# Kernel tuning notes

Hardware: AMD Instinct MI355X
Metric: run time of the kernel (lower is better)

## Reference

```python
import jax, jax.numpy as jnp
import numpy as np

NUM_USERS = 100000
NUM_ITEMS = 50000
NUM_EDGES = 4000000
EMB_DIM = 64
K_HOPS = 3


def setup_inputs() -> dict:
    key = jax.random.key(0)
    k1, k2, k3, k4, k5, k6 = jax.random.split(key, 6)
    N = NUM_USERS + NUM_ITEMS
    return {
        "users_emb": jax.random.normal(k1, (NUM_USERS, EMB_DIM), dtype=jnp.float32) * 0.1,
        "items_emb": jax.random.normal(k2, (NUM_ITEMS, EMB_DIM), dtype=jnp.float32) * 0.1,
        "edge_row": jax.random.randint(k3, (NUM_EDGES,), 0, N, dtype=jnp.int32),
        "edge_col": jax.random.randint(k4, (NUM_EDGES,), 0, N, dtype=jnp.int32),
        "user_id": jax.random.randint(k5, (4096,), 0, NUM_USERS, dtype=jnp.int32),
        "item_ids": jax.random.randint(k6, (4096,), 0, NUM_ITEMS, dtype=jnp.int32),
    }


def reference(users_emb, items_emb, edge_row, edge_col, user_id, item_ids):
    num_users = users_emb.shape[0]
    N = num_users + items_emb.shape[0]
    dt = users_emb.dtype

    # gcn_norm (no self loops): deg = rowsum of A, w_e = d_r^{-1/2} d_c^{-1/2}
    deg = jax.ops.segment_sum(jnp.ones(edge_row.shape[0], dtype=dt), edge_row,
                              num_segments=N)
    deg_inv_sqrt = jnp.where(deg > 0, 1.0 / jnp.sqrt(jnp.where(deg > 0, deg, 1.0)), 0.0)
    w = deg_inv_sqrt[edge_row] * deg_inv_sqrt[edge_col]  # [E]

    emb = jnp.concatenate([users_emb, items_emb], axis=0)  # [N, D]
    acc = emb  # running sum of K+1 layer snapshots
    for _ in range(K_HOPS):
        # SpMM: out[r] += w_e * emb[c]
        emb = jax.ops.segment_sum(w[:, None] * emb[edge_col], edge_row,
                                  num_segments=N)
        acc = acc + emb
    emb_final = acc / (K_HOPS + 1)  # layer-mean pooling

    users_final = emb_final[user_id]               # [B, D]
    items_final = emb_final[num_users + item_ids]  # [B, D]
    return jnp.concatenate([users_final, items_final], axis=1)  # [B, 2D]
```

## Files before the change

### kernel.cpp

```cpp
#include <hip/hip_runtime.h>
#include <hip/hip_bf16.h>

#define NUSERS 100000
#define NITEMS 50000
#define NN (NUSERS + NITEMS)
#define NE 4000000
#define DIM 64
#define BQ 4096
#define NBIN ((NN + 255) >> 8)
#define BINCAP 9216
#define EPB 4096

typedef unsigned short u16;
typedef unsigned int u32;
typedef float v2f __attribute__((ext_vector_type(2)));

__device__ __forceinline__ float bf2f(u16 u) {
    return __uint_as_float(((unsigned)u) << 16);
}
__device__ __forceinline__ u16 f2bf(float f) {
    unsigned x = __float_as_uint(f);
    return (u16)((x + 0x7FFFu + ((x >> 16) & 1u)) >> 16);
}
__device__ __forceinline__ void add8p(v2f* acc2, uint4 u) {
    acc2[0] += (v2f){__uint_as_float(u.x << 16), __uint_as_float(u.x & 0xffff0000u)};
    acc2[1] += (v2f){__uint_as_float(u.y << 16), __uint_as_float(u.y & 0xffff0000u)};
    acc2[2] += (v2f){__uint_as_float(u.z << 16), __uint_as_float(u.z & 0xffff0000u)};
    acc2[3] += (v2f){__uint_as_float(u.w << 16), __uint_as_float(u.w & 0xffff0000u)};
}
__device__ __forceinline__ uint4 ld_row(const char* __restrict__ base, int c, int dgoff) {
    u32 off = ((u32)c << 7) + (u32)dgoff;
    return *(const uint4*)(base + off);
}

__device__ __forceinline__ void rowsum_core(int start, int n8, int c_all,
                                            const int* __restrict__ col_s,
                                            const char* __restrict__ inb,
                                            int eslot, int dgoff, v2f* acc2) {
    int G = n8 >> 3;
    if (G <= 8) {
        int cg[8];
#pragma unroll
        for (int g = 0; g < 8; ++g)
            cg[g] = __shfl(c_all, (g << 3) + eslot, 64);
        uint4 v[8];
#pragma unroll
        for (int g = 0; g < 8; ++g)
            if (g < G) v[g] = ld_row(inb, cg[g], dgoff);
#pragma unroll
        for (int g = 0; g < 8; ++g)
            if (g < G) add8p(acc2, v[g]);
    } else {
        int i = eslot;
        int c0 = col_s[start + i];
        uint4 v0 = ld_row(inb, c0, dgoff);
        for (i += 8; i < n8; i += 8) {
            int c1 = col_s[start + i];
            uint4 v1 = ld_row(inb, c1, dgoff);
            add8p(acc2, v0);
            v0 = v1;
        }
        add8p(acc2, v0);
    }
}

__device__ __forceinline__ void reduce_acc(v2f* acc2) {
#pragma unroll
    for (int off = 8; off <= 32; off <<= 1)
#pragma unroll
        for (int j = 0; j < 4; ++j) {
            v2f o;
            o.x = __shfl_xor(acc2[j].x, off, 64);
            o.y = __shfl_xor(acc2[j].y, off, 64);
            acc2[j] += o;
        }
}

__global__ void k_init(int* __restrict__ bin_cur, u32* __restrict__ m2w,
                       u16* __restrict__ ea, u16* __restrict__ eb) {
    int t = blockIdx.x * blockDim.x + threadIdx.x;
    if (t < NBIN) bin_cur[t] = t * BINCAP;
    if (t < 37504) m2w[t] = 0;
    if (t < 32) {
        ((u32*)(ea + (size_t)NN * DIM))[t] = 0;
        ((u32*)(eb + (size_t)NN * DIM))[t] = 0;
    }
}

__global__ void k_binA(const int* __restrict__ row, const int* __restrict__ col,
                       int* __restrict__ bin_cur, u32* __restrict__ pairs, int E) {
    __shared__ int hist[NBIN];
    __shared__ int cbase[NBIN];
    int t = threadIdx.x;
    for (int b = t; b < NBIN; b += 256) hist[b] = 0;
    __syncthreads();
    int base = blockIdx.x * EPB;
    int r[16], c[16];
#pragma unroll
    for (int i = 0; i < 16; ++i) {
        int e = base + i * 256 + t;
        if (e < E) {
            r[i] = row[e];
            c[i] = col[e];
            atomicAdd(&hist[r[i] >> 8], 1);
        } else {
            r[i] = -1;
        }
    }
    __syncthreads();
    for (int b = t; b < NBIN; b += 256) {
        int h = hist[b];
        cbase[b] = (h > 0) ? atomicAdd(&bin_cur[b], h) : 0;
    }
    __syncthreads();
#pragma unroll
    for (int i = 0; i < 16; ++i) {
        if (r[i] >= 0) {
            int b = r[i] >> 8;
            int off = atomicSub(&hist[b], 1) - 1;
            pairs[(size_t)cbase[b] + off] = ((u32)(r[i] & 255) << 24) | (u32)c[i];
        }
    }
}

__global__ void k_binB(const u32* __restrict__ pairs, const int* __restrict__ bin_cur,
                       int* __restrict__ col_s, int* __restrict__ rs,
                       int* __restrict__ deg) {
    __shared__ int cnt[256];
    __shared__ int pscan[256];
    __shared__ int cur[256];
    int b = blockIdx.x;
    int t = threadIdx.x;
    int base = b * BINCAP;
    int end = bin_cur[b];
    cnt[t] = 0;
    __syncthreads();
    for (int i = base + t; i < end; i += 256)
        atomicAdd(&cnt[pairs[i] >> 24], 1);
    __syncthreads();
    int v = cnt[t];
    int pv = (v + 7) & ~7;
    pscan[t] = pv;
    __syncthreads();
    for (int off = 1; off < 256; off <<= 1) {
        int x = (t >= off) ? pscan[t - off] : 0;
        __syncthreads();
        pscan[t] += x;
        __syncthreads();
    }
    int rowstart = base + pscan[t] - pv;
    int r = (b << 8) + t;
    if (r < NN) {
        rs[r] = rowstart;
        deg[r] = v;
    }
    cur[t] = rowstart;
    for (int i = v; i < pv; ++i) col_s[rowstart + i] = NN;
    __syncthreads();
    for (int i = base + t; i < end; i += 256) {
        u32 p = pairs[i];
        int pos = atomicAdd(&cur[p >> 24], 1);
        col_s[pos] = (int)(p & 0x00FFFFFFu);
    }
}

__global__ void k_concat_t0(const float* __restrict__ u, const float* __restrict__ it,
                            const int* __restrict__ deg, u16* __restrict__ emb) {
    int i = blockIdx.x * blockDim.x + threadIdx.x;
    const int NU4 = NUSERS * DIM / 4;
    const int NT4 = NN * DIM / 4;
    if (i >= NT4) return;
    int row = i >> 4;
    int d = deg[row];
    float sc = (d > 0) ? (1.0f / sqrtf((float)d)) : 0.0f;
    float4 v = (i < NU4) ? ((const float4*)u)[i] : ((const float4*)it)[i - NU4];
    ushort4 o;
    o.x = f2bf(sc * v.x); o.y = f2bf(sc * v.y);
    o.z = f2bf(sc * v.z); o.w = f2bf(sc * v.w);
    ((ushort4*)emb)[i] = o;
}

__global__ void k_mark(const int* __restrict__ uid, const int* __restrict__ iid,
                       const int* __restrict__ rs, const int* __restrict__ deg,
                       const int* __restrict__ col_s, unsigned char* __restrict__ m2) {
    int q = blockIdx.x * blockDim.x + threadIdx.x;
    if (q >= 2 * BQ) return;
    int r = (q < BQ) ? uid[q] : (NUSERS + iid[q - BQ]);
    m2[r] = 1;
    int s = rs[r], n = deg[r];
    for (int i = 0; i < n; ++i) m2[col_s[s + i]] = 1;
}

__global__ void k_spmm8(const int* __restrict__ rs, const int* __restrict__ deg,
                        const int* __restrict__ col_s, const u16* __restrict__ in,
                        u16* __restrict__ out, const unsigned char* __restrict__ mask) {
    int wid = (blockIdx.x * blockDim.x + threadIdx.x) >> 6;
    if (wid >= NN) return;
    if (mask && !mask[wid]) return;
    int lane = threadIdx.x & 63;
    int eslot = lane >> 3;
    int dg = lane & 7;
    int dgoff = dg << 4;
    int n = deg[wid];
    int start = rs[wid];
    int n8 = (n + 7) & ~7;
    int c_all = col_s[start + lane];
    const char* inb = (const char*)in;
    v2f acc2[4] = {(v2f)0.f, (v2f)0.f, (v2f)0.f, (v2f)0.f};
    if (n8 > 0)
        rowsum_core(start, n8, c_all, col_s, inb, eslot, dgoff, acc2);
    reduce_acc(acc2);
    if (eslot == 0) {
        float s = (n > 0) ? (1.0f / (float)n) : 0.0f;
        v2f vs = {s, s};
        u32 p[4];
#pragma unroll
        for (int j = 0; j < 4; ++j) {
            v2f r = acc2[j] * vs;
            __hip_bfloat162 h = __float22bfloat162_rn(make_float2(r.x, r.y));
            p[j] = *(u32*)&h;
        }
        ((uint4*)out)[(size_t)wid * 8 + dg] = make_uint4(p[0], p[1], p[2], p[3]);
    }
}

__global__ void k_spmm_out(const int* __restrict__ rs, const int* __restrict__ deg,
                           const int* __restrict__ col_s, const u16* __restrict__ in,
                           const int* __restrict__ uid, const int* __restrict__ iid,
                           float* __restrict__ out) {
    int q = (blockIdx.x * blockDim.x + threadIdx.x) >> 6;
    if (q >= 2 * BQ) return;
    int lane = threadIdx.x & 63;
    int eslot = lane >> 3;
    int dg = lane & 7;
    int dgoff = dg << 4;
    int b, r, off;
    if (q < BQ) { b = q; r = uid[q]; off = 0; }
    else { b = q - BQ; r = NUSERS + iid[q - BQ]; off = DIM; }
    int n = deg[r];
    int start = rs[r];
    int n8 = (n + 7) & ~7;
    int c_all = col_s[start + lane];
    const char* inb = (const char*)in;
    v2f acc2[4] = {(v2f)0.f, (v2f)0.f, (v2f)0.f, (v2f)0.f};
    if (n8 > 0)
        rowsum_core(start, n8, c_all, col_s, inb, eslot, dgoff, acc2);
    reduce_acc(acc2);
    if (eslot == 0) {
        float dr = (n > 0) ? (1.0f / sqrtf((float)n)) : 0.0f;
        float* o = out + (size_t)b * (2 * DIM) + off + dg * 8;
#pragma unroll
        for (int j = 0; j < 4; ++j) {
            o[2 * j]     = (o[2 * j]     + dr * acc2[j].x) * 0.25f;
            o[2 * j + 1] = (o[2 * j + 1] + dr * acc2[j].y) * 0.25f;
        }
    }
}


__global__ void k_gather_init(const int* __restrict__ uid, const int* __restrict__ iid,
                              const float* __restrict__ u, const float* __restrict__ it,
                              float* __restrict__ out) {
    int t = blockIdx.x * blockDim.x + threadIdx.x;
    if (t >= BQ * DIM) return;
    int b = t >> 6;
    int d = t & 63;
    out[b * (2 * DIM) + d]       = u[(size_t)uid[b] * DIM + d];
    out[b * (2 * DIM) + DIM + d] = it[(size_t)iid[b] * DIM + d];
}

__global__ void k_gather_add(const int* __restrict__ uid, const int* __restrict__ iid,
                             const int* __restrict__ deg, const u16* __restrict__ emb,
                             float* __restrict__ out) {
    int t = blockIdx.x * blockDim.x + threadIdx.x;
    if (t >= BQ * DIM) return;
    int b = t >> 6;
    int d = t & 63;
    int ru = uid[b];
    int ri = NUSERS + iid[b];
    int du = deg[ru], di = deg[ri];
    float su = (du > 0) ? sqrtf((float)du) : 0.0f;
    float si = (di > 0) ? sqrtf((float)di) : 0.0f;
    int ou = b * (2 * DIM) + d;
    int oi = ou + DIM;
    out[ou] = out[ou] + su * bf2f(emb[(size_t)ru * DIM + d]);
    out[oi] = out[oi] + si * bf2f(emb[(size_t)ri * DIM + d]);
}


extern "C" void kernel_launch(void* const* d_in, const int* in_sizes, int n_in,
                              void* d_out, int out_size, void* d_ws, size_t ws_size,
                              hipStream_t stream) {
    const float* users_emb = (const float*)d_in[0];
    const float* items_emb = (const float*)d_in[1];
    const int*   edge_row  = (const int*)d_in[2];
    const int*   edge_col  = (const int*)d_in[3];
    const int*   user_id   = (const int*)d_in[4];
    const int*   item_ids  = (const int*)d_in[5];
    float* out = (float*)d_out;

    char* ws = (char*)d_ws;
    int*   deg_i   = (int*)  (ws + 0);
    int*   rs      = (int*)  (ws + 655360);
    int*   bin_cur = (int*)  (ws + 1310720);
    unsigned char* m2 = (unsigned char*)(ws + 1400000);
    int*   col_s   = (int*)  (ws + 4194304);
    u32*   pairs   = (u32*)  (ws + 29360128);
    u16*   emb_a   = (u16*)  (ws + 54525952);
    u16*   emb_b   = (u16*)  (ws + 75497472);

    k_init<<<147, 256, 0, stream>>>(bin_cur, (u32*)m2, emb_a, emb_b);

    k_binA<<<(NE + EPB - 1) / EPB, 256, 0, stream>>>(edge_row, edge_col, bin_cur, pairs, NE);
    k_binB<<<NBIN, 256, 0, stream>>>(pairs, bin_cur, col_s, rs, deg_i);

    k_concat_t0<<<(NN * DIM / 4 + 255) / 256, 256, 0, stream>>>(users_emb, items_emb,
                                                                deg_i, emb_a);

    k_gather_init<<<(BQ * DIM + 255) / 256, 256, 0, stream>>>(user_id, item_ids,
                                                              users_emb, items_emb, out);

    k_mark<<<(2 * BQ + 255) / 256, 256, 0, stream>>>(user_id, item_ids, rs, deg_i, col_s, m2);

    const int spmm_blocks = (NN + 3) / 4;
    k_spmm8<<<spmm_blocks, 256, 0, stream>>>(rs, deg_i, col_s, emb_a, emb_b,
                                             (const unsigned char*)nullptr);
    k_gather_add<<<(BQ * DIM + 255) / 256, 256, 0, stream>>>(user_id, item_ids, deg_i,
                                                             emb_b, out);
    k_spmm8<<<spmm_blocks, 256, 0, stream>>>(rs, deg_i, col_s, emb_b, emb_a, m2);
    k_gather_add<<<(BQ * DIM + 255) / 256, 256, 0, stream>>>(user_id, item_ids, deg_i,
                                                             emb_a, out);
    k_spmm_out<<<(2 * BQ + 3) / 4, 256, 0, stream>>>(rs, deg_i, col_s, emb_a,
                                                     user_id, item_ids, out);
}
```

Baseline: 356.1 us.

## Stage binned edges in LDS for coalesced scatter; parallelize mark per wavefront

The binning kernel now handles 16384 edges per block. It builds a local prefix-scanned histogram, stages the packed pairs in shared memory grouped by bin, and then writes each bin's run to global memory contiguously with wavefront-wide coalesced stores. This replaces the scattered per-edge global writes. The mark kernel gives one wavefront per query row instead of one thread, which spreads the neighbour loop across lanes. In exchange, the binning kernel uses much more shared memory (about 70KB), reads row twice, and launches far fewer blocks, which lowers occupancy.

New measurement: 356.3 us. About the same (+0.1%).

```diff
diff --git a/kernel.cpp b/kernel.cpp
--- a/kernel.cpp
+++ b/kernel.cpp
@@ -9,7 +9,7 @@
 #define BQ 4096
 #define NBIN ((NN + 255) >> 8)
 #define BINCAP 9216
-#define EPB 4096
+#define EPB2 16384
 
 typedef unsigned short u16;
 typedef unsigned int u32;
@@ -87,39 +87,66 @@
     }
 }
 
-__global__ void k_binA(const int* __restrict__ row, const int* __restrict__ col,
-                       int* __restrict__ bin_cur, u32* __restrict__ pairs, int E) {
+__global__ void k_binA2(const int* __restrict__ row, const int* __restrict__ col,
+                        int* __restrict__ bin_cur, u32* __restrict__ pairs, int E) {
+    __shared__ u32 stage[EPB2];
     __shared__ int hist[NBIN];
+    __shared__ int base_l[NBIN];
     __shared__ int cbase[NBIN];
+    __shared__ int lcur[NBIN];
+    __shared__ int tsum[256];
     int t = threadIdx.x;
+    int base = blockIdx.x * EPB2;
+    int lim = min(E - base, EPB2);
+
     for (int b = t; b < NBIN; b += 256) hist[b] = 0;
     __syncthreads();
-    int base = blockIdx.x * EPB;
-    int r[16], c[16];
-#pragma unroll
-    for (int i = 0; i < 16; ++i) {
-        int e = base + i * 256 + t;
-        if (e < E) {
-            r[i] = row[e];
-            c[i] = col[e];
-            atomicAdd(&hist[r[i] >> 8], 1);
-        } else {
-            r[i] = -1;
-        }
-    }
-    __syncthreads();
+
+    for (int i = t; i < lim; i += 256)
+        atomicAdd(&hist[row[base + i] >> 8], 1);
+    __syncthreads();
+
+    {
+        int b0 = t * 3;
+        int s0 = (b0 < NBIN) ? hist[b0] : 0;
+        int s1 = (b0 + 1 < NBIN) ? hist[b0 + 1] : 0;
+        int s2 = (b0 + 2 < NBIN) ? hist[b0 + 2] : 0;
+        int tot = s0 + s1 + s2;
+        tsum[t] = tot;
+        __syncthreads();
+        for (int off = 1; off < 256; off <<= 1) {
+            int x = (t >= off) ? tsum[t - off] : 0;
+            __syncthreads();
+            tsum[t] += x;
+            __syncthreads();
+        }
+        int excl = tsum[t] - tot;
+        if (b0 < NBIN)     { base_l[b0] = excl;           lcur[b0] = excl; }
+        if (b0 + 1 < NBIN) { base_l[b0 + 1] = excl + s0;  lcur[b0 + 1] = excl + s0; }
+        if (b0 + 2 < NBIN) { base_l[b0 + 2] = excl + s0 + s1; lcur[b0 + 2] = excl + s0 + s1; }
+    }
     for (int b = t; b < NBIN; b += 256) {
         int h = hist[b];
         cbase[b] = (h > 0) ? atomicAdd(&bin_cur[b], h) : 0;
     }
     __syncthreads();
-#pragma unroll
-    for (int i = 0; i < 16; ++i) {
-        if (r[i] >= 0) {
-            int b = r[i] >> 8;
-            int off = atomicSub(&hist[b], 1) - 1;
-            pairs[(size_t)cbase[b] + off] = ((u32)(r[i] & 255) << 24) | (u32)c[i];
-        }
+
+    for (int i = t; i < lim; i += 256) {
+        int r = row[base + i];
+        int c = col[base + i];
+        int pos = atomicAdd(&lcur[r >> 8], 1);
+        stage[pos] = ((u32)(r & 255) << 24) | (u32)c;
+    }
+    __syncthreads();
+
+    int wv = t >> 6;
+    int lane = t & 63;
+    for (int b = wv; b < NBIN; b += 4) {
+        int h = hist[b];
+        int lb = base_l[b];
+        int gb = cbase[b];
+        for (int i = lane; i < h; i += 64)
+            pairs[(size_t)gb + i] = stage[lb + i];
     }
 }
 
@@ -183,12 +210,13 @@
 __global__ void k_mark(const int* __restrict__ uid, const int* __restrict__ iid,
                        const int* __restrict__ rs, const int* __restrict__ deg,
                        const int* __restrict__ col_s, unsigned char* __restrict__ m2) {
-    int q = blockIdx.x * blockDim.x + threadIdx.x;
+    int q = (blockIdx.x * blockDim.x + threadIdx.x) >> 6;
     if (q >= 2 * BQ) return;
+    int lane = threadIdx.x & 63;
     int r = (q < BQ) ? uid[q] : (NUSERS + iid[q - BQ]);
-    m2[r] = 1;
+    if (lane == 0) m2[r] = 1;
     int s = rs[r], n = deg[r];
-    for (int i = 0; i < n; ++i) m2[col_s[s + i]] = 1;
+    for (int i = lane; i < n; i += 64) m2[col_s[s + i]] = 1;
 }
 
 __global__ void k_spmm8(const int* __restrict__ rs, const int* __restrict__ deg,
@@ -311,7 +339,8 @@
 
     k_init<<<147, 256, 0, stream>>>(bin_cur, (u32*)m2, emb_a, emb_b);
 
-    k_binA<<<(NE + EPB - 1) / EPB, 256, 0, stream>>>(edge_row, edge_col, bin_cur, pairs, NE);
+    k_binA2<<<(NE + EPB2 - 1) / EPB2, 256, 0, stream>>>(edge_row, edge_col, bin_cur,
+                                                        pairs, NE);
     k_binB<<<NBIN, 256, 0, stream>>>(pairs, bin_cur, col_s, rs, deg_i);
 
     k_concat_t0<<<(NN * DIM / 4 + 255) / 256, 256, 0, stream>>>(users_emb, items_emb,
@@ -320,7 +349,7 @@
     k_gather_init<<<(BQ * DIM + 255) / 256, 256, 0, stream>>>(user_id, item_ids,
                                                               users_emb, items_emb, out);
 
-    k_mark<<<(2 * BQ + 255) / 256, 256, 0, stream>>>(user_id, item_ids, rs, deg_i, col_s, m2);
+    k_mark<<<(2 * BQ + 3) / 4, 256, 0, stream>>>(user_id, item_ids, rs, deg_i, col_s, m2);
 
     const int spmm_blocks = (NN + 3) / 4;
     k_spmm8<<<spmm_blocks, 256, 0, stream>>>(rs, deg_i, col_s, emb_a, emb_b,
```
